# Kernel tuning notes

Measured on AMD Instinct MI355X. Metric: run time of the kernel, lower is better.

The kernel has to match this reference:

```python
import jax, jax.numpy as jnp
import numpy as np

N_NODES = 100000


def setup_inputs() -> dict:
    key = jax.random.key(0)
    ks = jax.random.split(key, 6)
    F_IN, F_CH, F_OUT = 64, 64, 64
    E = 1200000
    x = jax.random.normal(ks[0], (N_NODES, F_IN), dtype=jnp.float32)
    edge_index = jax.random.randint(ks[1], (2, E), 0, N_NODES, dtype=jnp.int64)
    # MLP params (PyTorch Linear default init scale ~ 1/sqrt(fan_in))
    s1 = 1.0 / np.sqrt(2 * F_IN)
    s2 = 1.0 / np.sqrt(F_CH)
    W1 = jax.random.uniform(ks[2], (2 * F_IN, F_CH), jnp.float32, -s1, s1)
    b1 = jax.random.uniform(ks[3], (F_CH,), jnp.float32, -s1, s1)
    W2 = jax.random.uniform(ks[4], (F_CH, F_OUT), jnp.float32, -s2, s2)
    b2 = jax.random.uniform(ks[5], (F_OUT,), jnp.float32, -s2, s2)
    return {"x": x, "edge_index": edge_index, "W1": W1, "b1": b1, "W2": W2, "b2": b2}


def reference(x, edge_index, W1, b1, W2, b2):
    # PyG EdgeConv with aggr='add': out_i = sum_j MLP(concat[x_i, x_j - x_i])
    src = edge_index[0]  # j (source / neighbor)
    dst = edge_index[1]  # i (target, aggregation index)
    x_i = x[dst]                     # [E, F]
    x_j = x[src]                     # [E, F]
    msg = jnp.concatenate([x_i, x_j - x_i], axis=-1)      # [E, 2F]
    h = jax.nn.relu(msg @ W1 + b1) @ W2 + b2               # [E, F_out]
    agg = jax.ops.segment_sum(h, dst, num_segments=N_NODES)  # [N, F_out]
    return jnp.tanh(agg)
```

## Files before the change

### kernel.cpp

```cpp
#include <hip/hip_runtime.h>
#include <math.h>


#define FDIM 64
#define BN 64
#define BSH 6
#define CAPB 1024
#define MAXB 2048
#define EPB 4096
#define XS_W 33
#define PRE_SMEM 24832

typedef unsigned int u32;
typedef unsigned short u16;
typedef _Float16 hf;

__device__ __forceinline__ float bf_lo(u32 u) {
    union { u32 i; float f; } c; c.i = u << 16; return c.f;
}
__device__ __forceinline__ float bf_hi(u32 u) {
    union { u32 i; float f; } c; c.i = u & 0xffff0000u; return c.f;
}
__device__ __forceinline__ u32 f2bf_rne(float f) {
    union { float f; u32 u; } c; c.f = f;
    u32 u = c.u;
    u += 0x7fffu + ((u >> 16) & 1u);
    return u >> 16;
}
__device__ __forceinline__ u32 f2h(float f) {
    union { u16 s; hf h; } c; c.h = (hf)f; return (u32)c.s;
}
__device__ __forceinline__ float h_lo(u32 u) {
    union { u16 s; hf h; } c; c.s = (u16)(u & 0xffffu); return (float)c.h;
}
__device__ __forceinline__ float h_hi(u32 u) {
    union { u16 s; hf h; } c; c.s = (u16)(u >> 16); return (float)c.h;
}

__global__ __launch_bounds__(256) void wprep_k(
    const float* __restrict__ W1, const float* __restrict__ W2,
    u32* __restrict__ Wchg, u32* __restrict__ W2hg)
{
    const int tid = threadIdx.x;
    for (int i = tid; i < 4096; i += 256) {
        int k = i >> 6, p = i & 63;
        u32 pk;
        if (p < 32) {
            int c = p * 2;
            float a0 = W1[k * 64 + c]     - W1[(64 + k) * 64 + c];
            float a1 = W1[k * 64 + c + 1] - W1[(64 + k) * 64 + c + 1];
            pk = f2h(a0) | (f2h(a1) << 16);
        } else {
            int c = (p - 32) * 2;
            pk = f2h(W1[(64 + k) * 64 + c]) | (f2h(W1[(64 + k) * 64 + c + 1]) << 16);
        }
        Wchg[i] = pk;
    }
    for (int i = tid; i < 2048; i += 256) {
        int k = i >> 5, c2 = i & 31;
        W2hg[i] = f2h(W2[k * 64 + c2 * 2]) | (f2h(W2[k * 64 + c2 * 2 + 1]) << 16);
    }
}

__global__ __launch_bounds__(256) void prep_k(
    const float* __restrict__ x, const u32* __restrict__ Wchg,
    const float* __restrict__ b1, u16* __restrict__ Ah,
    u16* __restrict__ Bmh, const int* __restrict__ ei,
    u32* __restrict__ slotB, int* __restrict__ gcnt,
    int N, int E, int NB, int nPre, int nBin)
{
    __shared__ __align__(16) char smem[PRE_SMEM];
    const int idx = blockIdx.x;
    const int tid = threadIdx.x;

    if ((idx % 6) == 5) {
        const int bb = idx / 6;
        if (bb >= nBin) return;
        int* histL = (int*)smem;
        int* gbase = histL + MAXB;
        const int e0 = bb * EPB;

        for (int j = tid; j < NB; j += 256) histL[j] = 0;
        __syncthreads();

        #pragma unroll
        for (int i = 0; i < EPB / 256; ++i) {
            int e = e0 + i * 256 + tid;
            if (e < E) {
                int d = ei[E + e];
                atomicAdd(&histL[d >> BSH], 1);
            }
        }
        __syncthreads();

        for (int j = tid; j < NB; j += 256) {
            int h = histL[j];
            gbase[j] = (h > 0) ? atomicAdd(&gcnt[j], h) : 0;
            histL[j] = 0;
        }
        __syncthreads();

        #pragma unroll
        for (int i = 0; i < EPB / 256; ++i) {
            int e = e0 + i * 256 + tid;
            if (e < E) {
                int s = ei[e];
                int d = ei[E + e];
                int b = d >> BSH;
                int pos = gbase[b] + atomicAdd(&histL[b], 1);
                if (pos < CAPB)
                    slotB[(size_t)b * CAPB + pos] =
                        ((u32)(d & (BN - 1)) << 20) | (u32)s;
            }
        }
        return;
    }

    const int pb = idx - idx / 6;
    if (pb >= nPre) return;
    u32 (*Wch)[64] = (u32(*)[64])smem;
    u32* xs = (u32*)(smem + 16384);

    const int node0 = pb * 64;

    {
        const uint4* Wg4 = (const uint4*)Wchg;
        #pragma unroll
        for (int it = 0; it < 4; ++it) {
            int i = it * 256 + tid;
            uint4 w = Wg4[i];
            *(uint4*)&Wch[i >> 4][(i & 15) * 4] = w;
        }
    }
    {
        const float4* X4 = (const float4*)x;
        #pragma unroll
        for (int it = 0; it < 4; ++it) {
            int i = it * 256 + tid;
            int n = i >> 4, k4 = i & 15;
            int gn = node0 + n;
            float4 v = make_float4(0.f, 0.f, 0.f, 0.f);
            if (gn < N) v = X4[(size_t)gn * 16 + k4];
            xs[n * XS_W + 2 * k4]     = f2h(v.x) | (f2h(v.y) << 16);
            xs[n * XS_W + 2 * k4 + 1] = f2h(v.z) | (f2h(v.w) << 16);
        }
    }
    __syncthreads();

    const int ng = tid & 15, cg = tid >> 4;
    const int n0 = ng * 4, c0 = cg * 8;
    const int wbase = (cg & 7) * 4 + ((cg >> 3) * 32);

    float acc[4][8];
    #pragma unroll
    for (int ci = 0; ci < 8; ++ci) {
        float init = b1[(c0 + ci) & 63];
        if (c0 >= 64) init = 0.f;
        #pragma unroll
        for (int ni = 0; ni < 4; ++ni) acc[ni][ci] = init;
    }

    #pragma unroll 4
    for (int kk = 0; kk < 32; ++kk) {
        u32 xv[4];
        #pragma unroll
        for (int ni = 0; ni < 4; ++ni) xv[ni] = xs[(n0 + ni) * XS_W + kk];
        uint4 w0 = *(const uint4*)&Wch[2 * kk][wbase];
        uint4 w1 = *(const uint4*)&Wch[2 * kk + 1][wbase];
        float ws0[8] = {h_lo(w0.x), h_hi(w0.x), h_lo(w0.y), h_hi(w0.y),
                        h_lo(w0.z), h_hi(w0.z), h_lo(w0.w), h_hi(w0.w)};
        float ws1[8] = {h_lo(w1.x), h_hi(w1.x), h_lo(w1.y), h_hi(w1.y),
                        h_lo(w1.z), h_hi(w1.z), h_lo(w1.w), h_hi(w1.w)};
        #pragma unroll
        for (int ni = 0; ni < 4; ++ni) {
            float xa = h_lo(xv[ni]);
            float xb = h_hi(xv[ni]);
            #pragma unroll
            for (int ci = 0; ci < 8; ++ci)
                acc[ni][ci] += xa * ws0[ci] + xb * ws1[ci];
        }
    }

    #pragma unroll
    for (int ni = 0; ni < 4; ++ni) {
        int n = node0 + n0 + ni;
        if (n >= N) break;
        if (c0 < 64) {
            uint4 pk;
            pk.x = f2h(acc[ni][0]) | (f2h(acc[ni][1]) << 16);
            pk.y = f2h(acc[ni][2]) | (f2h(acc[ni][3]) << 16);
            pk.z = f2h(acc[ni][4]) | (f2h(acc[ni][5]) << 16);
            pk.w = f2h(acc[ni][6]) | (f2h(acc[ni][7]) << 16);
            *(uint4*)&Ah[(size_t)n * 64 + c0] = pk;
        } else {
            uint4 pk;
            pk.x = f2bf_rne(acc[ni][0]) | (f2bf_rne(acc[ni][1]) << 16);
            pk.y = f2bf_rne(acc[ni][2]) | (f2bf_rne(acc[ni][3]) << 16);
            pk.z = f2bf_rne(acc[ni][4]) | (f2bf_rne(acc[ni][5]) << 16);
            pk.w = f2bf_rne(acc[ni][6]) | (f2bf_rne(acc[ni][7]) << 16);
            *(uint4*)&Bmh[(size_t)n * 64 + (c0 - 64)] = pk;
        }
    }
}

__device__ __forceinline__ float4 relu4add(float4 acc, float4 a, float4 b) {
    acc.x += fmaxf(a.x + b.x, 0.f);
    acc.y += fmaxf(a.y + b.y, 0.f);
    acc.z += fmaxf(a.z + b.z, 0.f);
    acc.w += fmaxf(a.w + b.w, 0.f);
    return acc;
}
__device__ __forceinline__ float4 relu4add_m(float4 acc, float4 a, float4 b, bool m) {
    acc.x += m ? fmaxf(a.x + b.x, 0.f) : 0.f;
    acc.y += m ? fmaxf(a.y + b.y, 0.f) : 0.f;
    acc.z += m ? fmaxf(a.z + b.z, 0.f) : 0.f;
    acc.w += m ? fmaxf(a.w + b.w, 0.f) : 0.f;
    return acc;
}
__device__ __forceinline__ float4 bf4(uint2 u) {
    return make_float4(bf_lo(u.x), bf_hi(u.x), bf_lo(u.y), bf_hi(u.y));
}

__global__ __launch_bounds__(256) void fused_agg(
    const u16* __restrict__ Ah, const u16* __restrict__ Bmh,
    const u32* __restrict__ slotB, const int* __restrict__ gcnt,
    const u32* __restrict__ W2hg, const float* __restrict__ b2,
    float* __restrict__ out, int N)
{
    __shared__ __align__(16) u32 W2h[64][34];
    __shared__ __align__(16) u32 pool[BN * 17 * 2];
    __shared__ u32 csrS[CAPB];
    __shared__ int histL[BN];
    __shared__ int rowO[BN + 1];
    __shared__ int ofs[BN];
    __shared__ float b2s[64];

    u32* eStage = pool;
    uint2* aggTb = (uint2*)pool;

    const int tid = threadIdx.x;
    const int b = blockIdx.x;
    const int node0 = b * BN;
    const int cntB = min(gcnt[b], CAPB);

    {
        const uint4* Wg4 = (const uint4*)W2hg;
        #pragma unroll
        for (int it = 0; it < 2; ++it) {
            int i = it * 256 + tid;
            uint4 w = Wg4[i];
            *(uint4*)&W2h[i >> 3][(i & 7) * 4] = w;
        }
    }
    if (tid < 64) b2s[tid] = b2[tid];
    if (tid < BN) histL[tid] = 0;
    __syncthreads();

    for (int i = tid; i < cntB; i += 256) {
        u32 e = slotB[(size_t)b * CAPB + i];
        eStage[i] = e;
        atomicAdd(&histL[e >> 20], 1);
    }
    __syncthreads();

    if (tid < 32) {
        int l = tid;
        int h0 = histL[2 * l], h1 = histL[2 * l + 1];
        int s = h0 + h1, inc = s;
        #pragma unroll
        for (int off = 1; off < 32; off <<= 1) {
            int t = __shfl_up(inc, off);
            if (l >= off) inc += t;
        }
        int base = inc - s;
        rowO[2 * l] = base; rowO[2 * l + 1] = base + h0;
        ofs[2 * l] = base;  ofs[2 * l + 1] = base + h0;
        if (l == 31) rowO[BN] = inc;
    }
    __syncthreads();

    for (int i = tid; i < cntB; i += 256) {
        u32 e = eStage[i];
        int pos = atomicAdd(&ofs[e >> 20], 1);
        csrS[pos] = e & 0xFFFFFu;
    }
    __syncthreads();

    {
        const int q = tid & 15, ng = tid >> 4;
        const uint2* __restrict__ B2 = (const uint2*)Bmh;
        const uint2* __restrict__ A2 = (const uint2*)Ah;
        #pragma unroll
        for (int h = 0; h < 4; ++h) {
            int nl = ng + h * 16;
            int gn = node0 + nl;
            int start = rowO[nl];
            int d = (gn < N) ? (rowO[nl + 1] - start) : 0;
            float4 a = make_float4(0.f, 0.f, 0.f, 0.f);
            if (gn < N) {
                uint2 ua = A2[(size_t)gn * 16 + q];
                a = make_float4(h_lo(ua.x), h_hi(ua.x), h_lo(ua.y), h_hi(ua.y));
            }
            float4 acc = make_float4(0.f, 0.f, 0.f, 0.f);

            int j = 0;
            for (; j + 8 <= d; j += 8) {
                int ss[8];
                uint2 bb[8];
                #pragma unroll
                for (int t = 0; t < 8; ++t) ss[t] = csrS[start + j + t];
                #pragma unroll
                for (int t = 0; t < 8; ++t) bb[t] = B2[(size_t)ss[t] * 16 + q];
                #pragma unroll
                for (int t = 0; t < 8; ++t) acc = relu4add(acc, a, bf4(bb[t]));
            }
            if (j < d) {
                int ss[8];
                uint2 bb[8];
                #pragma unroll
                for (int t = 0; t < 8; ++t) ss[t] = csrS[start + min(j + t, d - 1)];
                #pragma unroll
                for (int t = 0; t < 8; ++t) bb[t] = B2[(size_t)ss[t] * 16 + q];
                acc = relu4add(acc, a, bf4(bb[0]));
                #pragma unroll
                for (int t = 1; t < 8; ++t)
                    acc = relu4add_m(acc, a, bf4(bb[t]), j + t < d);
            }
            uint2 pk;
            pk.x = f2h(acc.x) | (f2h(acc.y) << 16);
            pk.y = f2h(acc.z) | (f2h(acc.w) << 16);
            aggTb[nl * 17 + q] = pk;
        }
    }
    __syncthreads();

    {
        const int cg = tid & 15, g = tid >> 4;
        const int c0 = cg * 4;
        const int nb0 = g * 4;
        float o[4][4];
        #pragma unroll
        for (int ni = 0; ni < 4; ++ni) {
            float dg = (float)(rowO[nb0 + ni + 1] - rowO[nb0 + ni]);
            #pragma unroll
            for (int ci = 0; ci < 4; ++ci) o[ni][ci] = dg * b2s[c0 + ci];
        }
        #pragma unroll 2
        for (int kc = 0; kc < 16; ++kc) {
            uint2 u0 = aggTb[(nb0 + 0) * 17 + kc];
            uint2 u1 = aggTb[(nb0 + 1) * 17 + kc];
            uint2 u2 = aggTb[(nb0 + 2) * 17 + kc];
            uint2 u3 = aggTb[(nb0 + 3) * 17 + kc];
            #pragma unroll
            for (int kk = 0; kk < 4; ++kk) {
                uint2 w2p = *(const uint2*)&W2h[kc * 4 + kk][cg * 2];
                float wv[4] = {h_lo(w2p.x), h_hi(w2p.x), h_lo(w2p.y), h_hi(w2p.y)};
                float a0 = (kk < 2) ? ((kk == 0) ? h_lo(u0.x) : h_hi(u0.x))
                                    : ((kk == 2) ? h_lo(u0.y) : h_hi(u0.y));
                float a1 = (kk < 2) ? ((kk == 0) ? h_lo(u1.x) : h_hi(u1.x))
                                    : ((kk == 2) ? h_lo(u1.y) : h_hi(u1.y));
                float a2 = (kk < 2) ? ((kk == 0) ? h_lo(u2.x) : h_hi(u2.x))
                                    : ((kk == 2) ? h_lo(u2.y) : h_hi(u2.y));
                float a3 = (kk < 2) ? ((kk == 0) ? h_lo(u3.x) : h_hi(u3.x))
                                    : ((kk == 2) ? h_lo(u3.y) : h_hi(u3.y));
                #pragma unroll
                for (int ci = 0; ci < 4; ++ci) {
                    o[0][ci] += a0 * wv[ci];
                    o[1][ci] += a1 * wv[ci];
                    o[2][ci] += a2 * wv[ci];
                    o[3][ci] += a3 * wv[ci];
                }
            }
        }
        #pragma unroll
        for (int ni = 0; ni < 4; ++ni) {
            int gn = node0 + nb0 + ni;
            if (gn < N) {
                float4 r = make_float4(tanhf(o[ni][0]), tanhf(o[ni][1]),
                                       tanhf(o[ni][2]), tanhf(o[ni][3]));
                ((float4*)out)[(size_t)gn * 16 + cg] = r;
            }
        }
    }
}

extern "C" void kernel_launch(void* const* d_in, const int* in_sizes, int n_in,
                              void* d_out, int out_size, void* d_ws, size_t ws_size,
                              hipStream_t stream)
{
    const float* x  = (const float*)d_in[0];
    const int*   ei = (const int*)d_in[1];
    const float* W1 = (const float*)d_in[2];
    const float* b1 = (const float*)d_in[3];
    const float* W2 = (const float*)d_in[4];
    const float* b2 = (const float*)d_in[5];
    float* out = (float*)d_out;

    const int N = in_sizes[0] / FDIM;
    const int E = in_sizes[1] / 2;
    const int NB = (N + BN - 1) / BN;

    u16*   Ah    = (u16*)d_ws;
    u16*   Bmh   = Ah + (size_t)N * FDIM;
    u32*   slotB = (u32*)(Bmh + (size_t)N * FDIM);
    u32*   Wchg  = slotB + (size_t)NB * CAPB;
    u32*   W2hg  = Wchg + 4096;
    int*   gcnt  = (int*)(W2hg + 2048);

    hipMemsetAsync(gcnt, 0, (size_t)NB * sizeof(int), stream);

    wprep_k<<<1, 256, 0, stream>>>(W1, W2, Wchg, W2hg);

    const int nPre = (N + 63) / 64;
    const int nBin = (E + EPB - 1) / EPB;
    int T = (nPre * 6 + 4) / 5;
    while (T - T / 6 < nPre) ++T;
    if (T < 6 * nBin) T = 6 * nBin;

    prep_k<<<T, 256, 0, stream>>>(x, Wchg, b1, Ah, Bmh, ei, slotB, gcnt,
                                  N, E, NB, nPre, nBin);
    fused_agg<<<NB, 256, 0, stream>>>(Ah, Bmh, slotB, gcnt, W2hg, b2, out, N);
}
```

Before: 186.6 us.

## Use fdot2 with k-pair packed weights and swizzled transposed x tile in prep

The node-side GEMM in prep_k now packs W1 and x as pairs along the k dimension, so each inner step runs a packed fp16 dot product (fdot2) with fp32 accumulation instead of converting halves to float and doing scalar FMAs. The x tile is stored transposed with an XOR swizzle, so each thread fetches its 4 nodes with one 128-bit shared load instead of four scalar loads. Separately, the edge-binning blocks now handle twice as many edges each, and the interleave ratio is changed from 1-in-6 to 1-in-11 blocks. This cuts instruction count and shared-memory traffic in the precompute, but the bin blocks become longer, which may hurt load balance.

```diff
diff --git a/kernel.cpp b/kernel.cpp
--- a/kernel.cpp
+++ b/kernel.cpp
@@ -7,13 +7,13 @@
 #define BSH 6
 #define CAPB 1024
 #define MAXB 2048
-#define EPB 4096
-#define XS_W 33
-#define PRE_SMEM 24832
+#define EPB 8192
+#define PRE_SMEM 24576
 
 typedef unsigned int u32;
 typedef unsigned short u16;
 typedef _Float16 hf;
+typedef _Float16 h2 __attribute__((ext_vector_type(2)));
 
 __device__ __forceinline__ float bf_lo(u32 u) {
     union { u32 i; float f; } c; c.i = u << 16; return c.f;
@@ -35,6 +35,9 @@
 }
 __device__ __forceinline__ float h_hi(u32 u) {
     union { u16 s; hf h; } c; c.s = (u16)(u >> 16); return (float)c.h;
+}
+__device__ __forceinline__ h2 u2h2(u32 u) {
+    union { u32 u; h2 h; } c; c.u = u; return c.h;
 }
 
 __global__ __launch_bounds__(256) void wprep_k(
@@ -43,18 +46,18 @@
 {
     const int tid = threadIdx.x;
     for (int i = tid; i < 4096; i += 256) {
-        int k = i >> 6, p = i & 63;
-        u32 pk;
-        if (p < 32) {
-            int c = p * 2;
-            float a0 = W1[k * 64 + c]     - W1[(64 + k) * 64 + c];
-            float a1 = W1[k * 64 + c + 1] - W1[(64 + k) * 64 + c + 1];
-            pk = f2h(a0) | (f2h(a1) << 16);
+        int kk = i >> 7, c = i & 127;
+        int k0 = 2 * kk, k1 = 2 * kk + 1;
+        float a0, a1;
+        if (c < 64) {
+            a0 = W1[k0 * 64 + c] - W1[(64 + k0) * 64 + c];
+            a1 = W1[k1 * 64 + c] - W1[(64 + k1) * 64 + c];
         } else {
-            int c = (p - 32) * 2;
-            pk = f2h(W1[(64 + k) * 64 + c]) | (f2h(W1[(64 + k) * 64 + c + 1]) << 16);
-        }
-        Wchg[i] = pk;
+            int cc = c - 64;
+            a0 = W1[(64 + k0) * 64 + cc];
+            a1 = W1[(64 + k1) * 64 + cc];
+        }
+        Wchg[i] = f2h(a0) | (f2h(a1) << 16);
     }
     for (int i = tid; i < 2048; i += 256) {
         int k = i >> 5, c2 = i & 31;
@@ -73,8 +76,8 @@
     const int idx = blockIdx.x;
     const int tid = threadIdx.x;
 
-    if ((idx % 6) == 5) {
-        const int bb = idx / 6;
+    if ((idx % 11) == 10) {
+        const int bb = idx / 11;
         if (bb >= nBin) return;
         int* histL = (int*)smem;
         int* gbase = histL + MAXB;
@@ -83,7 +86,7 @@
         for (int j = tid; j < NB; j += 256) histL[j] = 0;
         __syncthreads();
 
-        #pragma unroll
+        #pragma unroll 8
         for (int i = 0; i < EPB / 256; ++i) {
             int e = e0 + i * 256 + tid;
             if (e < E) {
@@ -100,7 +103,7 @@
         }
         __syncthreads();
 
-        #pragma unroll
+        #pragma unroll 8
         for (int i = 0; i < EPB / 256; ++i) {
             int e = e0 + i * 256 + tid;
             if (e < E) {
@@ -116,9 +119,9 @@
         return;
     }
 
-    const int pb = idx - idx / 6;
+    const int pb = idx - idx / 11;
     if (pb >= nPre) return;
-    u32 (*Wch)[64] = (u32(*)[64])smem;
+    u32 (*Wch)[128] = (u32(*)[128])smem;
     u32* xs = (u32*)(smem + 16384);
 
     const int node0 = pb * 64;
@@ -129,7 +132,7 @@
         for (int it = 0; it < 4; ++it) {
             int i = it * 256 + tid;
             uint4 w = Wg4[i];
-            *(uint4*)&Wch[i >> 4][(i & 15) * 4] = w;
+            *(uint4*)&Wch[i >> 5][(i & 31) * 4] = w;
         }
     }
     {
@@ -141,43 +144,39 @@
             int gn = node0 + n;
             float4 v = make_float4(0.f, 0.f, 0.f, 0.f);
             if (gn < N) v = X4[(size_t)gn * 16 + k4];
-            xs[n * XS_W + 2 * k4]     = f2h(v.x) | (f2h(v.y) << 16);
-            xs[n * XS_W + 2 * k4 + 1] = f2h(v.z) | (f2h(v.w) << 16);
+            int r0 = 2 * k4, r1 = 2 * k4 + 1;
+            int g = n >> 2, lo = n & 3;
+            xs[r0 * 64 + (((g ^ (r0 & 15)) << 2) | lo)] = f2h(v.x) | (f2h(v.y) << 16);
+            xs[r1 * 64 + (((g ^ (r1 & 15)) << 2) | lo)] = f2h(v.z) | (f2h(v.w) << 16);
         }
     }
     __syncthreads();
 
     const int ng = tid & 15, cg = tid >> 4;
     const int n0 = ng * 4, c0 = cg * 8;
-    const int wbase = (cg & 7) * 4 + ((cg >> 3) * 32);
 
     float acc[4][8];
     #pragma unroll
     for (int ci = 0; ci < 8; ++ci) {
-        float init = b1[(c0 + ci) & 63];
-        if (c0 >= 64) init = 0.f;
+        float init = (c0 < 64) ? b1[c0 + ci] : 0.f;
         #pragma unroll
         for (int ni = 0; ni < 4; ++ni) acc[ni][ci] = init;
     }
 
     #pragma unroll 4
     for (int kk = 0; kk < 32; ++kk) {
-        u32 xv[4];
-        #pragma unroll
-        for (int ni = 0; ni < 4; ++ni) xv[ni] = xs[(n0 + ni) * XS_W + kk];
-        uint4 w0 = *(const uint4*)&Wch[2 * kk][wbase];
-        uint4 w1 = *(const uint4*)&Wch[2 * kk + 1][wbase];
-        float ws0[8] = {h_lo(w0.x), h_hi(w0.x), h_lo(w0.y), h_hi(w0.y),
-                        h_lo(w0.z), h_hi(w0.z), h_lo(w0.w), h_hi(w0.w)};
-        float ws1[8] = {h_lo(w1.x), h_hi(w1.x), h_lo(w1.y), h_hi(w1.y),
-                        h_lo(w1.z), h_hi(w1.z), h_lo(w1.w), h_hi(w1.w)};
+        uint4 xq = *(const uint4*)&xs[kk * 64 + ((ng ^ (kk & 15)) << 2)];
+        uint4 w0 = *(const uint4*)&Wch[kk][c0];
+        uint4 w1 = *(const uint4*)&Wch[kk][c0 + 4];
+        h2 wv[8] = {u2h2(w0.x), u2h2(w0.y), u2h2(w0.z), u2h2(w0.w),
+                    u2h2(w1.x), u2h2(w1.y), u2h2(w1.z), u2h2(w1.w)};
+        u32 xv[4] = {xq.x, xq.y, xq.z, xq.w};
         #pragma unroll
         for (int ni = 0; ni < 4; ++ni) {
-            float xa = h_lo(xv[ni]);
-            float xb = h_hi(xv[ni]);
+            h2 xh = u2h2(xv[ni]);
             #pragma unroll
             for (int ci = 0; ci < 8; ++ci)
-                acc[ni][ci] += xa * ws0[ci] + xb * ws1[ci];
+                acc[ni][ci] = __builtin_amdgcn_fdot2(xh, wv[ci], acc[ni][ci], false);
         }
     }
 
@@ -413,9 +412,9 @@
 
     const int nPre = (N + 63) / 64;
     const int nBin = (E + EPB - 1) / EPB;
-    int T = (nPre * 6 + 4) / 5;
-    while (T - T / 6 < nPre) ++T;
-    if (T < 6 * nBin) T = 6 * nBin;
+    int T = (nPre * 11 + 9) / 10;
+    while (T - T / 11 < nPre) ++T;
+    if (T < 11 * nBin) T = 11 * nBin;
 
     prep_k<<<T, 256, 0, stream>>>(x, Wchg, b1, Ah, Bmh, ei, slotB, gcnt,
                                   N, E, NB, nPre, nBin);
```

Result: slower. 208.7 us (+11.8%).
